# Performance work log

Hardware: AMD Instinct MI355X
Metric: run time of the kernel (lower is better)

## Reference

```python
import jax, jax.numpy as jnp
import numpy as np

V, E, H, B, T, O = 32000, 512, 1024, 128, 512, 1
PAD_IDX = 0


def setup_inputs() -> dict:
    key = jax.random.key(0)
    ks = jax.random.split(key, 20)
    std = 1.0 / np.sqrt(H)
    u = lambda k, shape: jax.random.uniform(k, shape, jnp.float32, -std, std)
    inp = {
        "x": jax.random.randint(ks[0], (B, T), 0, V),
        "lengths": jax.random.randint(ks[1], (B,), 1, T + 1),
        "emb": jax.random.normal(ks[2], (V, E), jnp.float32),
        "W_ii": u(ks[3], (H, E)), "W_hi": u(ks[4], (H, H)), "b_i": u(ks[5], (H,)),
        "W_if": u(ks[6], (H, E)), "W_hf": u(ks[7], (H, H)), "b_f": u(ks[8], (H,)),
        "W_ig": u(ks[9], (H, E)), "W_hg": u(ks[10], (H, H)), "b_g": u(ks[11], (H,)),
        "W_io": u(ks[12], (H, E)), "W_ho": u(ks[13], (H, H)), "b_o": u(ks[14], (H,)),
        "fc_w": u(ks[15], (O, H)), "fc_b": u(ks[16], (O,)),
    }
    return inp


def reference(x, lengths, emb, W_ii, W_hi, b_i, W_if, W_hf, b_f,
              W_ig, W_hg, b_g, W_io, W_ho, b_o, fc_w, fc_b):
    # padding_idx row is frozen at zero (matches nn.Embedding(padding_idx=...))
    emb = emb.at[PAD_IDX].set(0.0)
    xe = emb[x]  # [B, T, E]

    # stack the 4 gate projections (same math, one GEMM): gate order i, f, g, o
    Wi = jnp.concatenate([W_ii, W_if, W_ig, W_io], axis=0)  # [4H, E]
    Wh = jnp.concatenate([W_hi, W_hf, W_hg, W_ho], axis=0)  # [4H, H]
    b = jnp.concatenate([b_i, b_f, b_g, b_o], axis=0)       # [4H]

    # precompute all input contributions in one big GEMM: [B, T, 4H]
    xp = jnp.einsum('bte,ge->btg', xe, Wi) + b
    xp_t = jnp.transpose(xp, (1, 0, 2))  # [T, B, 4H]

    h0 = jnp.zeros((B, H), jnp.float32)
    c0 = jnp.zeros((B, H), jnp.float32)
    out0 = jnp.zeros((B, H), jnp.float32)
    ts = jnp.arange(T)

    def step(carry, inputs):
        h, c, out = carry
        xpt, t = inputs
        z = xpt + h @ Wh.T  # [B, 4H]
        i_t = jax.nn.sigmoid(z[:, 0 * H:1 * H])
        f_t = jax.nn.sigmoid(z[:, 1 * H:2 * H])
        g_t = jnp.tanh(z[:, 2 * H:3 * H])
        o_t = jax.nn.sigmoid(z[:, 3 * H:4 * H])
        c = f_t * c + i_t * g_t
        h = o_t * jnp.tanh(c)
        mask = (lengths == t + 1)[:, None]  # [B, 1]
        out = jnp.where(mask, h, out)
        return (h, c, out), None

    (_, _, outputs), _ = jax.lax.scan(step, (h0, c0, out0), (xp_t, ts))
    return outputs @ fc_w.T + fc_b  # [B, O]
```

## Files before the change

kernel.cpp:

```cpp
#include <hip/hip_runtime.h>
#include <math.h>

#define Bsz 128
#define Tsz 512
#define Esz 512
#define Hsz 1024
#define G4H 4096
#define Vsz 32000
#define NB  64
#define BH  (Bsz * Hsz)
#define XPS 68

typedef __attribute__((ext_vector_type(8))) short short8;
typedef __attribute__((ext_vector_type(4))) short short4v;
typedef __attribute__((ext_vector_type(8))) __bf16 bf16x8;
typedef __attribute__((ext_vector_type(4))) float f32x4;
typedef __attribute__((ext_vector_type(4))) unsigned int uint4v;

__device__ inline unsigned short f2bf(float f) {
    unsigned u = __float_as_uint(f);
    u += 0x7fffu + ((u >> 16) & 1u);
    return (unsigned short)(u >> 16);
}
__device__ inline float bf2f(unsigned short s) {
    return __uint_as_float(((unsigned)s) << 16);
}
__device__ inline f32x4 mfma16(short8 a, short8 b, f32x4 c) {
    return __builtin_amdgcn_mfma_f32_16x16x32_bf16(
        __builtin_bit_cast(bf16x8, a), __builtin_bit_cast(bf16x8, b), c, 0, 0, 0);
}

#define GLD16P(dst, p)  asm volatile("global_load_dwordx4 %0, %1, off"         : "=&v"(dst) : "v"(p))
#define GLD16C(dst, p)  asm volatile("global_load_dwordx4 %0, %1, off sc0 sc1" : "=&v"(dst) : "v"(p))

#define WAITVM(n)                                                          \
    do { asm volatile("s_waitcnt vmcnt(" #n ")" ::: "memory");             \
         __builtin_amdgcn_sched_barrier(0); } while (0)

__device__ inline unsigned ld_flag(const unsigned* p) {
    unsigned r;
    asm volatile("global_load_dword %0, %1, off sc0 sc1\n\ts_waitcnt vmcnt(0)"
                 : "=&v"(r) : "v"(p) : "memory");
    return r;
}
__device__ inline void st_flag(unsigned* p, unsigned v) {
    asm volatile("global_store_dword %0, %1, off sc0 sc1" :: "v"(p), "v"(v) : "memory");
}

__global__ void k_prep_emb(const float* __restrict__ emb, unsigned short* __restrict__ dst) {
    size_t i = (size_t)blockIdx.x * 256 + threadIdx.x;
    if (i < (size_t)Vsz * Esz) dst[i] = f2bf(i < Esz ? 0.f : emb[i]);
}

__global__ void k_prep_w(const float* __restrict__ wi, const float* __restrict__ wf,
                         const float* __restrict__ wg, const float* __restrict__ wo,
                         int ncols, unsigned short* __restrict__ dst) {
    size_t i = (size_t)blockIdx.x * 256 + threadIdx.x;
    size_t per = (size_t)Hsz * ncols;
    if (i < 4 * per) {
        int g = (int)(i / per);
        size_t rem = i - (size_t)g * per;
        const float* src = g == 0 ? wi : g == 1 ? wf : g == 2 ? wg : wo;
        dst[i] = f2bf(src[rem]);
    }
}

__global__ void k_prep_misc(const float* __restrict__ bi, const float* __restrict__ bff,
                            const float* __restrict__ bg, const float* __restrict__ bo,
                            float* __restrict__ b4, unsigned short* __restrict__ ghbuf,
                            float* __restrict__ cbuf, float* __restrict__ outh,
                            unsigned* __restrict__ flags) {
    int i = blockIdx.x * 256 + threadIdx.x;
    if (i < G4H) {
        const float* src = i < Hsz ? bi : i < 2 * Hsz ? bff : i < 3 * Hsz ? bg : bo;
        b4[i] = src[i & (Hsz - 1)];
    }
    if (i < 2 * BH) ghbuf[i] = 0;
    if (i < BH) { cbuf[i] = 0.f; outh[i] = 0.f; }
    if (i < NB * 32) flags[i] = 0u;
}

__global__ __launch_bounds__(256, 2) void xp_gemm(
    const unsigned short* __restrict__ emb16, const unsigned short* __restrict__ Wi16,
    const float* __restrict__ b4, const int* __restrict__ x,
    unsigned short* __restrict__ xp, int t_base)
{
    const int tp = blockIdx.x;
    const int n0 = blockIdx.y * 128;
    const int tid = threadIdx.x;
    const int w = tid >> 6, l = tid & 63;
    const int wm = w >> 1, wn = w & 1;
    const int lr = l & 15, lk = l >> 4;

    const unsigned short* arow[4];
    #pragma unroll
    for (int mt = 0; mt < 4; ++mt) {
        int b = wm * 64 + mt * 16 + lr;
        int xv = x[b * Tsz + t_base + tp];
        arow[mt] = emb16 + (size_t)xv * Esz + lk * 8;
    }
    const unsigned short* brow[4];
    #pragma unroll
    for (int nt = 0; nt < 4; ++nt) {
        int n = n0 + wn * 64 + nt * 16 + lr;
        brow[nt] = Wi16 + (size_t)n * Esz + lk * 8;
    }
    f32x4 acc[4][4] = {};
    #pragma unroll 2
    for (int k0 = 0; k0 < Esz; k0 += 32) {
        short8 av[4], bv[4];
        #pragma unroll
        for (int mt = 0; mt < 4; ++mt) av[mt] = *(const short8*)(arow[mt] + k0);
        #pragma unroll
        for (int nt = 0; nt < 4; ++nt) bv[nt] = *(const short8*)(brow[nt] + k0);
        #pragma unroll
        for (int mt = 0; mt < 4; ++mt)
            #pragma unroll
            for (int nt = 0; nt < 4; ++nt)
                acc[mt][nt] = mfma16(av[mt], bv[nt], acc[mt][nt]);
    }
    #pragma unroll
    for (int nt = 0; nt < 4; ++nt) {
        int n = n0 + wn * 64 + nt * 16 + lr;
        float bias = b4[n];
        int g = n >> 10, j = n & 1023;
        int bk = j >> 4, jj = j & 15;
        #pragma unroll
        for (int mt = 0; mt < 4; ++mt) {
            #pragma unroll
            for (int r = 0; r < 4; ++r) {
                int b = wm * 64 + mt * 16 + lk * 4 + r;
                xp[((size_t)tp * NB + bk) * (Bsz * 64) + b * 64 + jj * 4 + g] =
                    f2bf(acc[mt][nt][r] + bias);
            }
        }
    }
}

__global__ __launch_bounds__(512, 1) void lstm_fused(
    const unsigned short* __restrict__ Wh16,
    const unsigned short* __restrict__ xpcur,
    unsigned short* __restrict__ xpnext,
    const unsigned short* __restrict__ emb16,
    const unsigned short* __restrict__ Wi16,
    const float* __restrict__ b4,
    const int* __restrict__ x,
    const int* __restrict__ lengths,
    unsigned short* __restrict__ ghbuf,
    float* __restrict__ cbuf,
    float* __restrict__ outh,
    unsigned* __restrict__ flags,
    int t0, int nsteps, int gt_base, int do_gemm)
{
    __shared__ unsigned short Whs[64][1032];
    __shared__ unsigned short xps[Bsz * XPS];
    __shared__ unsigned short hls[Bsz * 16];
    const int tid = threadIdx.x;
    const int blk = blockIdx.x;

    if (blk >= NB) {
        if (!do_gemm) return;
        const int gb = blk - NB;
        const int G = (int)gridDim.x - NB;
        const int w = tid >> 6, l = tid & 63;
        const int wm = w >> 2, wn = w & 3;
        const int lr = l & 15, lk = l >> 4;
        const int njobs = nsteps * 16;
        for (int job = gb; job < njobs; job += G) {
            int tp = job >> 4;
            int n0 = (job & 15) * 256;
            const unsigned short* arow[4];
            #pragma unroll
            for (int mt = 0; mt < 4; ++mt) {
                int b = wm * 64 + mt * 16 + lr;
                int xv = x[b * Tsz + gt_base + tp];
                arow[mt] = emb16 + (size_t)xv * Esz + lk * 8;
            }
            const unsigned short* brow[4];
            #pragma unroll
            for (int nt = 0; nt < 4; ++nt) {
                int n = n0 + wn * 64 + nt * 16 + lr;
                brow[nt] = Wi16 + (size_t)n * Esz + lk * 8;
            }
            f32x4 acc[4][4] = {};
            #pragma unroll 2
            for (int k0 = 0; k0 < Esz; k0 += 32) {
                short8 av[4], bv[4];
                #pragma unroll
                for (int mt = 0; mt < 4; ++mt) av[mt] = *(const short8*)(arow[mt] + k0);
                #pragma unroll
                for (int nt = 0; nt < 4; ++nt) bv[nt] = *(const short8*)(brow[nt] + k0);
                #pragma unroll
                for (int mt = 0; mt < 4; ++mt)
                    #pragma unroll
                    for (int nt = 0; nt < 4; ++nt)
                        acc[mt][nt] = mfma16(av[mt], bv[nt], acc[mt][nt]);
            }
            #pragma unroll
            for (int nt = 0; nt < 4; ++nt) {
                int n = n0 + wn * 64 + nt * 16 + lr;
                float bias = b4[n];
                int g = n >> 10, j = n & 1023;
                int bk = j >> 4, jj = j & 15;
                #pragma unroll
                for (int mt = 0; mt < 4; ++mt) {
                    #pragma unroll
                    for (int r = 0; r < 4; ++r) {
                        int b = wm * 64 + mt * 16 + lk * 4 + r;
                        xpnext[((size_t)tp * NB + bk) * (Bsz * 64) + b * 64 + jj * 4 + g] =
                            f2bf(acc[mt][nt][r] + bias);
                    }
                }
            }
        }
        return;
    }

    const int j0 = blk * 16;

    for (int idx = tid; idx < 64 * 128; idx += 512) {
        int n = idx >> 7, gq = idx & 127;
        int grow = (n >> 4) * Hsz + j0 + (n & 15);
        *(short8*)&Whs[n][gq << 3] =
            *(const short8*)(Wh16 + (size_t)grow * Hsz + gq * 8);
    }

    const int w = tid >> 6, l = tid & 63, lr = l & 15, lk = l >> 4;

    int lenr[4];
    float creg[4];
    #pragma unroll
    for (int r = 0; r < 4; ++r) {
        int b = 16 * w + 4 * lk + r;
        lenr[r] = lengths[b];
        creg[r] = cbuf[(size_t)b * Hsz + j0 + lr];
    }

    {
        const short8* sp = (const short8*)(xpcur + (size_t)blk * (Bsz * 64));
        int xb = tid >> 2, xq = tid & 3;
        *(short8*)&xps[xb * XPS + xq * 16]     = sp[tid * 2];
        *(short8*)&xps[xb * XPS + xq * 16 + 8] = sp[tid * 2 + 1];
    }
    __syncthreads();

    const int hb_off = (lk >> 1) * 2048 + (lk & 1) * 8 + (16 * w + lr) * 16;

#define ISSUE_CHUNK(buf, kc_) do {                                         \
        GLD16C(buf[0], hb + (kc_) * 16384 + 0);                            \
        GLD16C(buf[1], hb + (kc_) * 16384 + 4096);                         \
        GLD16C(buf[2], hb + (kc_) * 16384 + 8192);                         \
        GLD16C(buf[3], hb + (kc_) * 16384 + 12288);                        \
    } while (0)

#define CONSUME(buf, kc_) do {                                             \
        _Pragma("unroll")                                                  \
        for (int ks_ = 0; ks_ < 4; ++ks_) {                                \
            short8 a_ = __builtin_bit_cast(short8, buf[ks_]);              \
            const int go_ = ((kc_) * 16 + ks_ * 4 + lk) << 3;              \
            _Pragma("unroll")                                              \
            for (int nt_ = 0; nt_ < 4; ++nt_) {                            \
                short8 bv_ = *(const short8*)&Whs[nt_ * 16 + lr][go_];     \
                acc[nt_] = mfma16(a_, bv_, acc[nt_]);                      \
            }                                                              \
        }                                                                  \
    } while (0)

    for (int s = 0; s < nsteps; ++s) {
        const int t = t0 + s;
        const unsigned short* hb = ghbuf + (size_t)(t & 1) * BH + hb_off;
        int sn = (s + 1 < nsteps) ? s + 1 : s;
        const unsigned short* xpn = xpcur + ((size_t)sn * NB + blk) * (Bsz * 64) + tid * 16;

        f32x4 acc[4] = {};
        uint4v P[4], Q[4], R[4], S[4], xr0, xr1;
        ISSUE_CHUNK(P, 0); ISSUE_CHUNK(Q, 1); ISSUE_CHUNK(R, 2); ISSUE_CHUNK(S, 3);
        WAITVM(12); CONSUME(P, 0); ISSUE_CHUNK(P, 4);
        WAITVM(12); CONSUME(Q, 1); ISSUE_CHUNK(Q, 5);
        WAITVM(12); CONSUME(R, 2); ISSUE_CHUNK(R, 6);
        WAITVM(12); CONSUME(S, 3); ISSUE_CHUNK(S, 7);
        WAITVM(12); CONSUME(P, 4);
        GLD16P(xr0, xpn); GLD16P(xr1, xpn + 8);
        WAITVM(10); CONSUME(Q, 5);
        WAITVM(6);  CONSUME(R, 6);
        WAITVM(2);  CONSUME(S, 7);

        #pragma unroll
        for (int r = 0; r < 4; ++r) {
            int b = 16 * w + 4 * lk + r;
            short4v xg4 = *(const short4v*)&xps[b * XPS + lr * 4];
            float zi = acc[0][r] + bf2f((unsigned short)xg4[0]);
            float zf = acc[1][r] + bf2f((unsigned short)xg4[1]);
            float zg = acc[2][r] + bf2f((unsigned short)xg4[2]);
            float zo = acc[3][r] + bf2f((unsigned short)xg4[3]);
            float it = 1.f / (1.f + __expf(-zi));
            float ft = 1.f / (1.f + __expf(-zf));
            float gt = tanhf(zg);
            float ot = 1.f / (1.f + __expf(-zo));
            float c = ft * creg[r] + it * gt;
            creg[r] = c;
            float h = ot * tanhf(c);
            if (lenr[r] == t + 1) outh[(size_t)b * Hsz + j0 + lr] = h;
            hls[b * 16 + lr] = f2bf(h);
        }
        __syncthreads();

        unsigned short* ghn = ghbuf + (size_t)((t + 1) & 1) * BH;
        if (tid < 256) {
            short8 hv8 = *(const short8*)&hls[tid * 8];
            unsigned short* hd = ghn + (size_t)blk * 2048 + tid * 8;
            asm volatile("global_store_dwordx4 %0, %1, off sc0 sc1"
                         :: "v"(hd), "v"(__builtin_bit_cast(uint4v, hv8)) : "memory");
        }

        WAITVM(0);
        {
            int xb = tid >> 2, xq = tid & 3;
            *(short8*)&xps[xb * XPS + xq * 16]     = __builtin_bit_cast(short8, xr0);
            *(short8*)&xps[xb * XPS + xq * 16 + 8] = __builtin_bit_cast(short8, xr1);
        }
        __syncthreads();

        if (tid == 0) st_flag(&flags[blk * 32], (unsigned)(t + 1));
        {
            const unsigned* fp = &flags[(tid & 63) * 32];
            while (ld_flag(fp) < (unsigned)(t + 1)) __builtin_amdgcn_s_sleep(1);
        }
        __syncthreads();
        __builtin_amdgcn_sched_barrier(0);
    }

    #pragma unroll
    for (int r = 0; r < 4; ++r) {
        int b = 16 * w + 4 * lk + r;
        cbuf[(size_t)b * Hsz + j0 + lr] = creg[r];
    }
#undef ISSUE_CHUNK
#undef CONSUME
}

__global__ __launch_bounds__(64) void k_fc(const float* __restrict__ outh,
                                           const float* __restrict__ fc_w,
                                           const float* __restrict__ fc_b,
                                           float* __restrict__ out) {
    int b = blockIdx.x, l = threadIdx.x;
    float s = 0.f;
    for (int k = l; k < Hsz; k += 64) s += outh[(size_t)b * Hsz + k] * fc_w[k];
    #pragma unroll
    for (int o = 32; o > 0; o >>= 1) s += __shfl_down(s, o);
    if (l == 0) out[b] = s + fc_b[0];
}

extern "C" void kernel_launch(void* const* d_in, const int* in_sizes, int n_in,
                              void* d_out, int out_size, void* d_ws, size_t ws_size,
                              hipStream_t stream) {
    const int* x       = (const int*)d_in[0];
    const int* lengths = (const int*)d_in[1];
    const float* emb   = (const float*)d_in[2];
    const float* W_ii  = (const float*)d_in[3];
    const float* W_hi  = (const float*)d_in[4];
    const float* b_i   = (const float*)d_in[5];
    const float* W_if  = (const float*)d_in[6];
    const float* W_hf  = (const float*)d_in[7];
    const float* b_f   = (const float*)d_in[8];
    const float* W_ig  = (const float*)d_in[9];
    const float* W_hg  = (const float*)d_in[10];
    const float* b_g   = (const float*)d_in[11];
    const float* W_io  = (const float*)d_in[12];
    const float* W_ho  = (const float*)d_in[13];
    const float* b_o   = (const float*)d_in[14];
    const float* fc_w  = (const float*)d_in[15];
    const float* fc_b  = (const float*)d_in[16];
    float* out = (float*)d_out;

    char* ws = (char*)d_ws;
    size_t off = 0;
    auto take = [&](size_t bytes) { size_t o = off; off += (bytes + 255) & ~(size_t)255; return o; };
    unsigned* flags       = (unsigned*)(ws + take((size_t)NB * 128));
    unsigned short* ghbuf = (unsigned short*)(ws + take((size_t)2 * BH * 2));
    float* cbuf           = (float*)(ws + take((size_t)BH * 4));
    float* outh           = (float*)(ws + take((size_t)BH * 4));
    float* b4             = (float*)(ws + take((size_t)G4H * 4));
    unsigned short* Wi16  = (unsigned short*)(ws + take((size_t)G4H * Esz * 2));
    unsigned short* Wh16  = (unsigned short*)(ws + take((size_t)G4H * Hsz * 2));
    unsigned short* emb16 = (unsigned short*)(ws + take((size_t)Vsz * Esz * 2));
    size_t fixed = off;

    int TC = 128;
    while (TC > 1 && fixed + 2 * ((size_t)TC * Bsz * G4H * 2 + 256) > ws_size) TC >>= 1;
    unsigned short* xp0 = (unsigned short*)(ws + take((size_t)TC * Bsz * G4H * 2));
    unsigned short* xp1 = (unsigned short*)(ws + take((size_t)TC * Bsz * G4H * 2));
    unsigned short* xpb[2] = {xp0, xp1};

    k_prep_emb<<<(Vsz * Esz + 255) / 256, 256, 0, stream>>>(emb, emb16);
    k_prep_w<<<(4 * Hsz * Esz + 255) / 256, 256, 0, stream>>>(W_ii, W_if, W_ig, W_io, Esz, Wi16);
    k_prep_w<<<(4 * Hsz * Hsz + 255) / 256, 256, 0, stream>>>(W_hi, W_hf, W_hg, W_ho, Hsz, Wh16);
    k_prep_misc<<<(2 * BH + 255) / 256, 256, 0, stream>>>(b_i, b_f, b_g, b_o, b4, ghbuf, cbuf, outh, flags);

    const int nch = Tsz / TC;
    {
        dim3 g(TC, G4H / 128);
        xp_gemm<<<g, 256, 0, stream>>>(emb16, Wi16, b4, x, xp0, 0);
    }
    for (int c = 0; c < nch; ++c) {
        lstm_fused<<<256, 512, 0, stream>>>(
            Wh16, xpb[c & 1], xpb[(c + 1) & 1], emb16, Wi16, b4, x,
            lengths, ghbuf, cbuf, outh, flags,
            c * TC, TC, (c + 1) * TC, (c + 1 < nch) ? 1 : 0);
    }
    k_fc<<<Bsz, 64, 0, stream>>>(outh, fc_w, fc_b, out);
}
```

Measured before the change: 3.986 ms.

## Use uneven chunk schedule, load gate inputs directly, and spin on flags with one wave

Timesteps are split into uneven chunks: a short first chunk of 16 steps lets the recurrent kernel start sooner after the initial input-projection GEMM, and later chunks of 64 steps keep the GEMM overlapped on the spare blocks. Each step now loads its precomputed gate inputs straight into registers with small global loads, replacing the shared-memory staging and the prefetch for the next step. The flag barrier polls with only the first wave, using a wave-wide all-reduce, instead of having every thread spin. The cost is an extra global load latency on the critical path of each step, and a fixed 64-step buffer size that no longer adapts to the workspace size.

After: 3.918 ms. No clear change (-1.7%).

```diff
diff --git a/kernel.cpp b/kernel.cpp
--- a/kernel.cpp
+++ b/kernel.cpp
@@ -9,13 +9,13 @@
 #define Vsz 32000
 #define NB  64
 #define BH  (Bsz * Hsz)
-#define XPS 68
 
 typedef __attribute__((ext_vector_type(8))) short short8;
 typedef __attribute__((ext_vector_type(4))) short short4v;
 typedef __attribute__((ext_vector_type(8))) __bf16 bf16x8;
 typedef __attribute__((ext_vector_type(4))) float f32x4;
 typedef __attribute__((ext_vector_type(4))) unsigned int uint4v;
+typedef __attribute__((ext_vector_type(2))) unsigned int uint2v;
 
 __device__ inline unsigned short f2bf(float f) {
     unsigned u = __float_as_uint(f);
@@ -31,6 +31,7 @@
 }
 
 #define GLD16P(dst, p)  asm volatile("global_load_dwordx4 %0, %1, off"         : "=&v"(dst) : "v"(p))
+#define GLD8P(dst, p)   asm volatile("global_load_dwordx2 %0, %1, off"         : "=&v"(dst) : "v"(p))
 #define GLD16C(dst, p)  asm volatile("global_load_dwordx4 %0, %1, off sc0 sc1" : "=&v"(dst) : "v"(p))
 
 #define WAITVM(n)                                                          \
@@ -150,22 +151,21 @@
     float* __restrict__ cbuf,
     float* __restrict__ outh,
     unsigned* __restrict__ flags,
-    int t0, int nsteps, int gt_base, int do_gemm)
+    int t0, int nsteps, int gt_base, int gn)
 {
     __shared__ unsigned short Whs[64][1032];
-    __shared__ unsigned short xps[Bsz * XPS];
     __shared__ unsigned short hls[Bsz * 16];
     const int tid = threadIdx.x;
     const int blk = blockIdx.x;
 
     if (blk >= NB) {
-        if (!do_gemm) return;
+        if (gn == 0) return;
         const int gb = blk - NB;
         const int G = (int)gridDim.x - NB;
         const int w = tid >> 6, l = tid & 63;
         const int wm = w >> 2, wn = w & 3;
         const int lr = l & 15, lk = l >> 4;
-        const int njobs = nsteps * 16;
+        const int njobs = gn * 16;
         for (int job = gb; job < njobs; job += G) {
             int tp = job >> 4;
             int n0 = (job & 15) * 256;
@@ -235,16 +235,10 @@
         lenr[r] = lengths[b];
         creg[r] = cbuf[(size_t)b * Hsz + j0 + lr];
     }
-
-    {
-        const short8* sp = (const short8*)(xpcur + (size_t)blk * (Bsz * 64));
-        int xb = tid >> 2, xq = tid & 3;
-        *(short8*)&xps[xb * XPS + xq * 16]     = sp[tid * 2];
-        *(short8*)&xps[xb * XPS + xq * 16 + 8] = sp[tid * 2 + 1];
-    }
     __syncthreads();
 
     const int hb_off = (lk >> 1) * 2048 + (lk & 1) * 8 + (16 * w + lr) * 16;
+    const int xg_off = (16 * w + 4 * lk) * 64 + lr * 4;
 
 #define ISSUE_CHUNK(buf, kc_) do {                                         \
         GLD16C(buf[0], hb + (kc_) * 16384 + 0);                            \
@@ -269,26 +263,31 @@
     for (int s = 0; s < nsteps; ++s) {
         const int t = t0 + s;
         const unsigned short* hb = ghbuf + (size_t)(t & 1) * BH + hb_off;
-        int sn = (s + 1 < nsteps) ? s + 1 : s;
-        const unsigned short* xpn = xpcur + ((size_t)sn * NB + blk) * (Bsz * 64) + tid * 16;
+        const unsigned short* xgp = xpcur + (size_t)s * (NB * Bsz * 64)
+                                  + (size_t)blk * (Bsz * 64) + xg_off;
+
+        uint2v xg[4];
+        GLD8P(xg[0], xgp + 0);
+        GLD8P(xg[1], xgp + 64);
+        GLD8P(xg[2], xgp + 128);
+        GLD8P(xg[3], xgp + 192);
 
         f32x4 acc[4] = {};
-        uint4v P[4], Q[4], R[4], S[4], xr0, xr1;
+        uint4v P[4], Q[4], R[4], S[4];
         ISSUE_CHUNK(P, 0); ISSUE_CHUNK(Q, 1); ISSUE_CHUNK(R, 2); ISSUE_CHUNK(S, 3);
         WAITVM(12); CONSUME(P, 0); ISSUE_CHUNK(P, 4);
         WAITVM(12); CONSUME(Q, 1); ISSUE_CHUNK(Q, 5);
         WAITVM(12); CONSUME(R, 2); ISSUE_CHUNK(R, 6);
         WAITVM(12); CONSUME(S, 3); ISSUE_CHUNK(S, 7);
         WAITVM(12); CONSUME(P, 4);
-        GLD16P(xr0, xpn); GLD16P(xr1, xpn + 8);
-        WAITVM(10); CONSUME(Q, 5);
-        WAITVM(6);  CONSUME(R, 6);
-        WAITVM(2);  CONSUME(S, 7);
+        WAITVM(8);  CONSUME(Q, 5);
+        WAITVM(4);  CONSUME(R, 6);
+        WAITVM(0);  CONSUME(S, 7);
 
         #pragma unroll
         for (int r = 0; r < 4; ++r) {
             int b = 16 * w + 4 * lk + r;
-            short4v xg4 = *(const short4v*)&xps[b * XPS + lr * 4];
+            short4v xg4 = __builtin_bit_cast(short4v, xg[r]);
             float zi = acc[0][r] + bf2f((unsigned short)xg4[0]);
             float zf = acc[1][r] + bf2f((unsigned short)xg4[1]);
             float zg = acc[2][r] + bf2f((unsigned short)xg4[2]);
@@ -312,19 +311,18 @@
             asm volatile("global_store_dwordx4 %0, %1, off sc0 sc1"
                          :: "v"(hd), "v"(__builtin_bit_cast(uint4v, hv8)) : "memory");
         }
-
         WAITVM(0);
-        {
-            int xb = tid >> 2, xq = tid & 3;
-            *(short8*)&xps[xb * XPS + xq * 16]     = __builtin_bit_cast(short8, xr0);
-            *(short8*)&xps[xb * XPS + xq * 16 + 8] = __builtin_bit_cast(short8, xr1);
-        }
         __syncthreads();
 
         if (tid == 0) st_flag(&flags[blk * 32], (unsigned)(t + 1));
-        {
-            const unsigned* fp = &flags[(tid & 63) * 32];
-            while (ld_flag(fp) < (unsigned)(t + 1)) __builtin_amdgcn_s_sleep(1);
+        if (tid < 64) {
+            const unsigned* fp = &flags[tid * 32];
+            unsigned tgt = (unsigned)(t + 1);
+            unsigned v = ld_flag(fp);
+            while (!__all((int)(v >= tgt))) {
+                __builtin_amdgcn_s_sleep(1);
+                v = ld_flag(fp);
+            }
         }
         __syncthreads();
         __builtin_amdgcn_sched_barrier(0);
@@ -384,12 +382,10 @@
     unsigned short* Wi16  = (unsigned short*)(ws + take((size_t)G4H * Esz * 2));
     unsigned short* Wh16  = (unsigned short*)(ws + take((size_t)G4H * Hsz * 2));
     unsigned short* emb16 = (unsigned short*)(ws + take((size_t)Vsz * Esz * 2));
-    size_t fixed = off;
-
-    int TC = 128;
-    while (TC > 1 && fixed + 2 * ((size_t)TC * Bsz * G4H * 2 + 256) > ws_size) TC >>= 1;
-    unsigned short* xp0 = (unsigned short*)(ws + take((size_t)TC * Bsz * G4H * 2));
-    unsigned short* xp1 = (unsigned short*)(ws + take((size_t)TC * Bsz * G4H * 2));
+
+    const int TCcap = 64;
+    unsigned short* xp0 = (unsigned short*)(ws + take((size_t)TCcap * Bsz * G4H * 2));
+    unsigned short* xp1 = (unsigned short*)(ws + take((size_t)TCcap * Bsz * G4H * 2));
     unsigned short* xpb[2] = {xp0, xp1};
 
     k_prep_emb<<<(Vsz * Esz + 255) / 256, 256, 0, stream>>>(emb, emb16);
@@ -397,16 +393,21 @@
     k_prep_w<<<(4 * Hsz * Hsz + 255) / 256, 256, 0, stream>>>(W_hi, W_hf, W_hg, W_ho, Hsz, Wh16);
     k_prep_misc<<<(2 * BH + 255) / 256, 256, 0, stream>>>(b_i, b_f, b_g, b_o, b4, ghbuf, cbuf, outh, flags);
 
-    const int nch = Tsz / TC;
+    const int bounds[11] = {0, 16, 48, 112, 176, 240, 304, 368, 432, 496, 512};
+    const int nch = 10;
+
     {
-        dim3 g(TC, G4H / 128);
+        dim3 g(bounds[1], 32);
         xp_gemm<<<g, 256, 0, stream>>>(emb16, Wi16, b4, x, xp0, 0);
     }
-    for (int c = 0; c < nch; ++c) {
+    for (int i = 0; i < nch; ++i) {
+        int t0b = bounds[i], ns = bounds[i + 1] - bounds[i];
+        int gtb = bounds[i + 1];
+        int gn = (i + 1 < nch) ? bounds[i + 2] - bounds[i + 1] : 0;
         lstm_fused<<<256, 512, 0, stream>>>(
-            Wh16, xpb[c & 1], xpb[(c + 1) & 1], emb16, Wi16, b4, x,
+            Wh16, xpb[i & 1], xpb[(i + 1) & 1], emb16, Wi16, b4, x,
             lengths, ghbuf, cbuf, outh, flags,
-            c * TC, TC, (c + 1) * TC, (c + 1 < nch) ? 1 : 0);
+            t0b, ns, gtb, gn);
     }
     k_fc<<<Bsz, 64, 0, stream>>>(outh, fc_w, fc_b, out);
 }
```
